# Performance work log

Hardware: AMD Instinct MI355X
Metric: run time of the kernel (lower is better)

## Reference

```python
import jax, jax.numpy as jnp
import numpy as np

BATCH = 4096      # batch_size per the module __init__
TEMP = 0.5        # temperature
WORLD = 1         # world_size (single device; GatherLayer path skipped)
D = 128           # projection-head embedding dim
EPS = 1e-8        # torch CosineSimilarity eps


def _neg_indices(N, half):
    # Static mask from mask_correlated_samples: remove diagonal and the
    # (i, half+i)/(half+i, i) entries; each row keeps exactly N-2 columns.
    mask = np.ones((N, N), dtype=bool)
    np.fill_diagonal(mask, False)
    r = np.arange(half)
    mask[r, half + r] = False
    mask[half + r, r] = False
    return np.nonzero(mask)[1].reshape(N, N - 2)  # row-major -> per-row sorted cols


def setup_inputs() -> dict:
    key = jax.random.key(0)
    k1, k2 = jax.random.split(key)
    z_i = jax.random.normal(k1, (BATCH, D), dtype=jnp.float32)
    z_j = jax.random.normal(k2, (BATCH, D), dtype=jnp.float32)
    return {"z_i": z_i, "z_j": z_j}


def reference(z_i, z_j):
    half = BATCH * WORLD
    N = 2 * half
    z = jnp.concatenate([z_i, z_j], axis=0)                       # (N, D)
    zn = z / jnp.maximum(jnp.linalg.norm(z, axis=1, keepdims=True), EPS)
    # reordered_z = cat(z[half:], z[:half]) == roll by -half
    rn = jnp.roll(zn, -half, axis=0)
    # cosine-sim matrix via single GEMM instead of (N,1,D)x(1,N,D) broadcast
    sim = (zn @ rn.T) / TEMP                                       # (N, N)

    i = jnp.arange(half)
    sim_i_j = sim[i, i + half]          # torch.diag(sim, +half)
    sim_j_i = sim[i + half, i]          # torch.diag(sim, -half)
    pos = jnp.concatenate([sim_i_j, sim_j_i])[:, None]             # (N, 1)

    neg_idx = jnp.asarray(_neg_indices(N, half))                   # (N, N-2) static
    neg = jnp.take_along_axis(sim, neg_idx, axis=1)                # (N, N-2)

    logits = jnp.concatenate([pos, neg], axis=1)                   # (N, N-1)
    # CrossEntropy with labels=0, reduction='sum', then / N
    loss = jnp.sum(jax.nn.logsumexp(logits, axis=1) - logits[:, 0]) / N
    return loss
```

## Files before the change

### kernel.cpp

```cpp
#include <hip/hip_runtime.h>

#define HALF   4096
#define NROWS  8192
#define DDIM   128
#define NGROUPS (NROWS / 128)
#define NPAIRS  (NGROUPS * (NGROUPS + 1) / 2)
#define LDS_STRIDE 272

typedef _Float16 v8h __attribute__((ext_vector_type(8)));
typedef _Float16 v2h __attribute__((ext_vector_type(2)));
typedef float    v4f __attribute__((ext_vector_type(4)));

#if __has_builtin(__builtin_amdgcn_exp2f)
#define EXP2F(x) __builtin_amdgcn_exp2f(x)
#else
#define EXP2F(x) exp2f(x)
#endif
#if __has_builtin(__builtin_amdgcn_logf)
#define LOG2F(x) __builtin_amdgcn_logf(x)
#else
#define LOG2F(x) __log2f(x)
#endif

#define CEXP 2.8853900817779268f

__global__ __launch_bounds__(256) void nt_normalize(
        const float* __restrict__ z_i, const float* __restrict__ z_j,
        _Float16* __restrict__ zn, float* __restrict__ S, float* __restrict__ acc) {
    int tid  = threadIdx.x;
    int lane = tid & 63;
    int row  = blockIdx.x * 4 + (tid >> 6);
    if (tid < 4) S[blockIdx.x * 4 + tid] = 0.f;
    if (blockIdx.x == 0 && tid == 4) acc[0] = 0.f;

    const float* src = (row < HALF) ? (z_i + (size_t)row * DDIM)
                                    : (z_j + (size_t)(row - HALF) * DDIM);
    float2 v = *(const float2*)(src + lane * 2);
    float ss = v.x * v.x + v.y * v.y;
    #pragma unroll
    for (int off = 32; off >= 1; off >>= 1)
        ss += __shfl_xor(ss, off, 64);
    float inv = 1.0f / fmaxf(sqrtf(ss), 1e-8f);
    v2h p;
    p.x = (_Float16)(v.x * inv);
    p.y = (_Float16)(v.y * inv);
    *(v2h*)(zn + (size_t)row * DDIM + lane * 2) = p;
}

__global__ __launch_bounds__(256, 4) void nt_gram_sym(
        const _Float16* __restrict__ zn, float* __restrict__ S) {
    __shared__ unsigned char lds[128 * LDS_STRIDE];

    int tid  = threadIdx.x;
    int lane = tid & 63;
    int w    = tid >> 6;
    int quad = lane >> 4;
    int cl   = lane & 15;

    int p = blockIdx.x;
    int J = (int)((sqrtf(8.0f * (float)p + 1.0f) - 1.0f) * 0.5f);
    while ((J + 1) * (J + 2) / 2 <= p) ++J;
    while (J * (J + 1) / 2 > p) --J;
    int I = p - J * (J + 1) / 2;
    int r0 = I * 128, c0 = J * 128;
    bool offdiag = (I != J);

    v8h a[2][4];
    #pragma unroll
    for (int u = 0; u < 2; ++u) {
        int arow = r0 + w * 32 + u * 16 + cl;
        #pragma unroll
        for (int t = 0; t < 4; ++t)
            a[u][t] = *(const v8h*)(zn + (size_t)arow * DDIM + t * 32 + quad * 8);
    }

    const uint4* gb = (const uint4*)zn;
    #pragma unroll
    for (int i = 0; i < 8; ++i) {
        int rr = (tid >> 4) + i * 16;
        uint4 v = gb[(size_t)(c0 + rr) * 16 + (tid & 15)];
        *(uint4*)&lds[(size_t)rr * LDS_STRIDE + (tid & 15) * 16] = v;
    }
    __syncthreads();

    float sums[2][4] = {{0.f,0.f,0.f,0.f},{0.f,0.f,0.f,0.f}};

    #pragma unroll
    for (int sub = 0; sub < 8; ++sub) {
        v4f acc0 = {0.f, 0.f, 0.f, 0.f};
        v4f acc1 = {0.f, 0.f, 0.f, 0.f};
        #pragma unroll
        for (int t = 0; t < 4; ++t) {
            v8h b = *(const v8h*)&lds[(size_t)(sub * 16 + cl) * LDS_STRIDE + t * 64 + quad * 16];
            acc0 = __builtin_amdgcn_mfma_f32_16x16x32_f16(a[0][t], b, acc0, 0, 0, 0);
            acc1 = __builtin_amdgcn_mfma_f32_16x16x32_f16(a[1][t], b, acc1, 0, 0, 0);
        }
        float cp = 0.f;
        #pragma unroll
        for (int r = 0; r < 4; ++r) {
            float e0 = EXP2F(fmaf(acc0[r], CEXP, -CEXP));
            float e1 = EXP2F(fmaf(acc1[r], CEXP, -CEXP));
            sums[0][r] += e0;
            sums[1][r] += e1;
            cp += e0 + e1;
        }
        if (offdiag) {
            cp += __shfl_xor(cp, 16, 64);
            cp += __shfl_xor(cp, 32, 64);
            if (quad == 0)
                atomicAdd(&S[c0 + sub * 16 + cl], cp);
        }
    }

    #pragma unroll
    for (int u = 0; u < 2; ++u)
        #pragma unroll
        for (int r = 0; r < 4; ++r) {
            float s = sums[u][r];
            #pragma unroll
            for (int off = 1; off < 16; off <<= 1)
                s += __shfl_xor(s, off, 64);
            if (cl == 0)
                atomicAdd(&S[r0 + w * 32 + u * 16 + quad * 4 + r], s);
        }
}

__global__ __launch_bounds__(256) void nt_correct(
        const _Float16* __restrict__ zn, const float* __restrict__ S,
        float* __restrict__ acc) {
    int tid  = threadIdx.x;
    int lane = tid & 63;
    int w    = tid >> 6;

    float part = 0.f;
    #pragma unroll 1
    for (int q = 0; q < 16; ++q) {
        int pr = (blockIdx.x * 4 + w) * 16 + q;
        v2h xa = *(const v2h*)(zn + (size_t)pr * DDIM + lane * 2);
        v2h xb = *(const v2h*)(zn + (size_t)(pr + HALF) * DDIM + lane * 2);
        float d = (float)xa.x * (float)xb.x + (float)xa.y * (float)xb.y;
        #pragma unroll
        for (int off = 32; off >= 1; off >>= 1)
            d += __shfl_xor(d, off, 64);
        if (lane == 0) {
            float e = EXP2F(fmaf(d, CEXP, -CEXP));
            part += LOG2F(S[pr] - e) + LOG2F(S[pr + HALF] - e);
        }
    }

    __shared__ float red[4];
    if (lane == 0) red[w] = part;
    __syncthreads();
    if (tid == 0)
        atomicAdd(acc, red[0] + red[1] + red[2] + red[3]);
}

__global__ void nt_final(const float* __restrict__ acc, float* __restrict__ out) {
    out[0] = acc[0] * (0.69314718055994531f / (float)NROWS);
}

extern "C" void kernel_launch(void* const* d_in, const int* in_sizes, int n_in,
                              void* d_out, int out_size, void* d_ws, size_t ws_size,
                              hipStream_t stream) {
    const float* z_i = (const float*)d_in[0];
    const float* z_j = (const float*)d_in[1];
    _Float16* zn  = (_Float16*)d_ws;
    float*    S   = (float*)((char*)d_ws + (size_t)NROWS * DDIM * 2);
    float*    acc = S + NROWS;
    float*    out = (float*)d_out;

    nt_normalize<<<dim3(NROWS / 4), dim3(256), 0, stream>>>(z_i, z_j, zn, S, acc);
    nt_gram_sym<<<dim3(NPAIRS), dim3(256), 0, stream>>>(zn, S);
    nt_correct<<<dim3(HALF / 64), dim3(256), 0, stream>>>(zn, S, acc);
    nt_final<<<dim3(1), dim3(1), 0, stream>>>(acc, out);
}
```

Measured before the change: 94.45 us.

## Capture positive-pair exps in Gram kernel, reduce column atomics, merge final kernels

The Gram kernel now writes the positive-pair exponentials straight from the diagonal of the I,I+32 tiles into a buffer P. The correction kernel therefore no longer reloads zn or recomputes the dot products. Column partial sums are combined across the four waves in LDS before one atomic per column, so each tile issues a quarter as many column atomics. The correction and final-scale kernels become a single 1024-thread block that writes the output directly, removing one launch and the acc buffer. The cost is a single-block reduction and an extra branch inside the Gram inner loop.

```diff
diff --git a/kernel.cpp b/kernel.cpp
--- a/kernel.cpp
+++ b/kernel.cpp
@@ -26,12 +26,11 @@
 
 __global__ __launch_bounds__(256) void nt_normalize(
         const float* __restrict__ z_i, const float* __restrict__ z_j,
-        _Float16* __restrict__ zn, float* __restrict__ S, float* __restrict__ acc) {
+        _Float16* __restrict__ zn, float* __restrict__ S) {
     int tid  = threadIdx.x;
     int lane = tid & 63;
     int row  = blockIdx.x * 4 + (tid >> 6);
     if (tid < 4) S[blockIdx.x * 4 + tid] = 0.f;
-    if (blockIdx.x == 0 && tid == 4) acc[0] = 0.f;
 
     const float* src = (row < HALF) ? (z_i + (size_t)row * DDIM)
                                     : (z_j + (size_t)(row - HALF) * DDIM);
@@ -48,8 +47,10 @@
 }
 
 __global__ __launch_bounds__(256, 4) void nt_gram_sym(
-        const _Float16* __restrict__ zn, float* __restrict__ S) {
+        const _Float16* __restrict__ zn, float* __restrict__ S,
+        float* __restrict__ P) {
     __shared__ unsigned char lds[128 * LDS_STRIDE];
+    __shared__ float cs[4][128];
 
     int tid  = threadIdx.x;
     int lane = tid & 63;
@@ -64,6 +65,7 @@
     int I = p - J * (J + 1) / 2;
     int r0 = I * 128, c0 = J * 128;
     bool offdiag = (I != J);
+    bool ppart   = (J == I + 32);
 
     v8h a[2][4];
     #pragma unroll
@@ -103,12 +105,16 @@
             sums[0][r] += e0;
             sums[1][r] += e1;
             cp += e0 + e1;
+            if (ppart && cl == quad * 4 + r) {
+                if (sub == w * 2)     P[r0 + w * 32 +      quad * 4 + r] = e0;
+                if (sub == w * 2 + 1) P[r0 + w * 32 + 16 + quad * 4 + r] = e1;
+            }
         }
         if (offdiag) {
             cp += __shfl_xor(cp, 16, 64);
             cp += __shfl_xor(cp, 32, 64);
             if (quad == 0)
-                atomicAdd(&S[c0 + sub * 16 + cl], cp);
+                cs[w][sub * 16 + cl] = cp;
         }
     }
 
@@ -123,40 +129,39 @@
             if (cl == 0)
                 atomicAdd(&S[r0 + w * 32 + u * 16 + quad * 4 + r], s);
         }
+
+    if (offdiag) {
+        __syncthreads();
+        if (tid < 128) {
+            float c = cs[0][tid] + cs[1][tid] + cs[2][tid] + cs[3][tid];
+            atomicAdd(&S[c0 + tid], c);
+        }
+    }
 }
 
-__global__ __launch_bounds__(256) void nt_correct(
-        const _Float16* __restrict__ zn, const float* __restrict__ S,
-        float* __restrict__ acc) {
-    int tid  = threadIdx.x;
-    int lane = tid & 63;
-    int w    = tid >> 6;
-
+__global__ __launch_bounds__(1024) void nt_correct(
+        const float* __restrict__ S, const float* __restrict__ P,
+        float* __restrict__ out) {
+    int tid = threadIdx.x;
     float part = 0.f;
-    #pragma unroll 1
-    for (int q = 0; q < 16; ++q) {
-        int pr = (blockIdx.x * 4 + w) * 16 + q;
-        v2h xa = *(const v2h*)(zn + (size_t)pr * DDIM + lane * 2);
-        v2h xb = *(const v2h*)(zn + (size_t)(pr + HALF) * DDIM + lane * 2);
-        float d = (float)xa.x * (float)xb.x + (float)xa.y * (float)xb.y;
+    #pragma unroll
+    for (int k = 0; k < 4; ++k) {
+        int pr = tid + k * 1024;
+        float e = P[pr];
+        part += LOG2F(S[pr] - e) + LOG2F(S[pr + HALF] - e);
+    }
+    #pragma unroll
+    for (int off = 32; off >= 1; off >>= 1)
+        part += __shfl_xor(part, off, 64);
+    __shared__ float red[16];
+    if ((tid & 63) == 0) red[tid >> 6] = part;
+    __syncthreads();
+    if (tid == 0) {
+        float t = 0.f;
         #pragma unroll
-        for (int off = 32; off >= 1; off >>= 1)
-            d += __shfl_xor(d, off, 64);
-        if (lane == 0) {
-            float e = EXP2F(fmaf(d, CEXP, -CEXP));
-            part += LOG2F(S[pr] - e) + LOG2F(S[pr + HALF] - e);
-        }
+        for (int i = 0; i < 16; ++i) t += red[i];
+        out[0] = t * (0.69314718055994531f / (float)NROWS);
     }
-
-    __shared__ float red[4];
-    if (lane == 0) red[w] = part;
-    __syncthreads();
-    if (tid == 0)
-        atomicAdd(acc, red[0] + red[1] + red[2] + red[3]);
-}
-
-__global__ void nt_final(const float* __restrict__ acc, float* __restrict__ out) {
-    out[0] = acc[0] * (0.69314718055994531f / (float)NROWS);
 }
 
 extern "C" void kernel_launch(void* const* d_in, const int* in_sizes, int n_in,
@@ -166,11 +171,10 @@
     const float* z_j = (const float*)d_in[1];
     _Float16* zn  = (_Float16*)d_ws;
     float*    S   = (float*)((char*)d_ws + (size_t)NROWS * DDIM * 2);
-    float*    acc = S + NROWS;
+    float*    P   = S + NROWS;
     float*    out = (float*)d_out;
 
-    nt_normalize<<<dim3(NROWS / 4), dim3(256), 0, stream>>>(z_i, z_j, zn, S, acc);
-    nt_gram_sym<<<dim3(NPAIRS), dim3(256), 0, stream>>>(zn, S);
-    nt_correct<<<dim3(HALF / 64), dim3(256), 0, stream>>>(zn, S, acc);
-    nt_final<<<dim3(1), dim3(1), 0, stream>>>(acc, out);
+    nt_normalize<<<dim3(NROWS / 4), dim3(256), 0, stream>>>(z_i, z_j, zn, S);
+    nt_gram_sym<<<dim3(NPAIRS), dim3(256), 0, stream>>>(zn, S, P);
+    nt_correct<<<dim3(1), dim3(1024), 0, stream>>>(S, P, out);
 }
```

Measured after the change: 82.29 us. 1.15x faster.
